# Kernel tuning notes

Hardware: AMD Instinct MI355X
Metric: run time of the kernel (lower is better)

## Reference

```python
import jax, jax.numpy as jnp
import numpy as np

N, M, E, DIM, H = 50000, 50000, 640000, 128, 8
DH = DIM // H
EPS = 1e-5

def _prelu(x, alpha):
    return jnp.where(x >= 0, x, alpha * x)

def setup_inputs() -> dict:
    key0 = jax.random.key(0)
    ks = jax.random.split(key0, 12)
    s = 1.0 / np.sqrt(DIM)
    return {
        "query": jax.random.normal(ks[0], (N, DIM), jnp.float32),
        "key": jax.random.normal(ks[1], (M, DIM), jnp.float32),
        "value": jax.random.normal(ks[2], (M, DIM), jnp.float32),
        "query_idx": jax.random.randint(ks[3], (E,), 0, N),
        "key_idx": jax.random.randint(ks[4], (E,), 0, M),
        "Wq": jax.random.normal(ks[5], (DIM, DIM), jnp.float32) * s,
        "bq": jnp.zeros((DIM,), jnp.float32),
        "Wk": jax.random.normal(ks[6], (DIM, DIM), jnp.float32) * s,
        "bk": jnp.zeros((DIM,), jnp.float32),
        "Wv": jax.random.normal(ks[7], (DIM, DIM), jnp.float32) * s,
        "bv": jnp.zeros((DIM,), jnp.float32),
        "Wp": jax.random.normal(ks[8], (DIM, DIM), jnp.float32) * s,
        "bp": jnp.zeros((DIM,), jnp.float32),
        "a": jax.random.normal(ks[9], (1, H, DH), jnp.float32) * 0.1,
        "alpha": jnp.full((1,), 0.25, jnp.float32),
        "gamma": jnp.ones((DIM,), jnp.float32),
        "beta": jnp.zeros((DIM,), jnp.float32),
    }

def reference(query, key, value, query_idx, key_idx, Wq, bq, Wk, bk, Wv, bv, Wp, bp, a, alpha, gamma, beta):
    n = query.shape[0]
    # projections (node-level, then gather per edge; linear commutes with gather)
    Qq = query @ Wq + bq            # [N, DIM]
    Kq = query @ Wk + bk            # [N, DIM] (self-attn key)
    Kk = key @ Wk + bk              # [M, DIM]
    Vq = query @ Wv + bv            # [N, DIM]
    Vv = value @ Wv + bv            # [M, DIM]
    # self-attention score per query node: [N, H, 1]
    attn_qq = (a * _prelu(Qq + Kq, alpha).reshape(n, H, DH)).sum(-1, keepdims=True)
    # per-edge additive attention score: [E, H, 1]
    e_feat = _prelu(Qq[query_idx] + Kk[key_idx], alpha)
    attn_e = (a * e_feat.reshape(-1, H, DH)).sum(-1, keepdims=True)
    # stable softmax over irregular query groups (include self)
    max_attn = jax.lax.stop_gradient(attn_qq.at[query_idx].max(attn_e))
    exp_qq = jnp.exp(attn_qq - max_attn)                 # [N, H, 1]
    exp_e = jnp.exp(attn_e - max_attn[query_idx])        # [E, H, 1]
    denom = exp_qq.at[query_idx].add(exp_e)              # [N, H, 1]
    denom = jnp.where(denom == 0, 1.0, denom)
    # weighted value scatter-sum (value_idx == key_idx)
    msg = exp_qq * Vq.reshape(n, H, DH)
    msg = msg.at[query_idx].add(exp_e * Vv[key_idx].reshape(-1, H, DH))
    out = (msg / denom).reshape(n, DIM) @ Wp + bp
    res = query + out
    mu = res.mean(-1, keepdims=True)
    var = res.var(-1, keepdims=True)
    return gamma * (res - mu) / jnp.sqrt(var + EPS) + beta
```

## Files before the change

### kernel.cpp

```cpp
#include <hip/hip_runtime.h>
#include <math.h>

#define DIM 128
#define NH 8
#define LN_EPS 1e-5f

using bf16x8 = __attribute__((ext_vector_type(8))) short;
using f32x4  = __attribute__((ext_vector_type(4))) float;

__device__ __forceinline__ float prelu_f(float x, float al) { return x >= 0.f ? x : al * x; }

__device__ __forceinline__ short f2bf(float f) {
    unsigned u = __float_as_uint(f);
    unsigned r = (u + 0x7fffu + ((u >> 16) & 1u)) >> 16;
    return (short)r;
}
__device__ __forceinline__ float bflo(unsigned u) { return __uint_as_float(u << 16); }
__device__ __forceinline__ float bfhi(unsigned u) { return __uint_as_float(u & 0xffff0000u); }

__device__ __forceinline__ unsigned cvt_pk_bf16(float lo, float hi) {
    unsigned r;
    asm("v_cvt_pk_bf16_f32 %0, %1, %2" : "=v"(r) : "v"(lo), "v"(hi));
    return r;
}

__device__ __forceinline__ float swz_xor1(float x) {
    return __int_as_float(__builtin_amdgcn_ds_swizzle(__float_as_int(x), 0x041F));
}
__device__ __forceinline__ float swz_xor2(float x) {
    return __int_as_float(__builtin_amdgcn_ds_swizzle(__float_as_int(x), 0x081F));
}
__device__ __forceinline__ float swz_xor4(float x) {
    return __int_as_float(__builtin_amdgcn_ds_swizzle(__float_as_int(x), 0x101F));
}
__device__ __forceinline__ float swz_xor8(float x) {
    return __int_as_float(__builtin_amdgcn_ds_swizzle(__float_as_int(x), 0x201F));
}

__global__ __launch_bounds__(256) void pack_w_kernel(
    const float* __restrict__ W0, const float* __restrict__ W1,
    const float* __restrict__ W2, const float* __restrict__ W3,
    short* __restrict__ P0, short* __restrict__ P1,
    short* __restrict__ P2, short* __restrict__ P3)
{
    const int id = blockIdx.x * 256 + threadIdx.x;
    const int mat = id >> 11;
    const int rem = id & 2047;
    const int ks = rem >> 9;
    const int ct = (rem >> 6) & 7;
    const int lane = rem & 63;
    const int lr = lane & 15, lg = lane >> 4;
    const float* W = mat == 0 ? W0 : mat == 1 ? W1 : mat == 2 ? W2 : W3;
    short* P = mat == 0 ? P0 : mat == 1 ? P1 : mat == 2 ? P2 : P3;
    short v[8];
    #pragma unroll
    for (int r = 0; r < 8; ++r)
        v[r] = f2bf(W[(ks * 32 + lg * 8 + r) * DIM + ct * 16 + lr]);
    *(bf16x8*)&P[(size_t)((ks * 8 + ct) * 64 + lane) * 8] = *(bf16x8*)v;
}

__global__ __launch_bounds__(256) void proj_query_mfma(
    const float* __restrict__ query,
    const short* __restrict__ Wqp, const short* __restrict__ Wkp, const short* __restrict__ Wvp,
    const float* __restrict__ bq, const float* __restrict__ bk, const float* __restrict__ bv,
    const float* __restrict__ avec, const float* __restrict__ alpha_p,
    float* __restrict__ QV32, float* __restrict__ attnqq, int N)
{
    __shared__ float lds[4][16][130];
    const int wid = threadIdx.x >> 6, lane = threadIdx.x & 63;
    const int row0 = (blockIdx.x * 4 + wid) * 16;
    if (row0 >= N) return;
    const int lr = lane & 15, lg = lane >> 4;

    bf16x8 afrag[4];
    const int arow = row0 + lr;
    const bool rowok = arow < N;
    #pragma unroll
    for (int ks = 0; ks < 4; ++ks) {
        float t[8] = {0.f,0.f,0.f,0.f,0.f,0.f,0.f,0.f};
        if (rowok) {
            *(float4*)&t[0] = *(const float4*)&query[(size_t)arow * DIM + ks * 32 + lg * 8];
            *(float4*)&t[4] = *(const float4*)&query[(size_t)arow * DIM + ks * 32 + lg * 8 + 4];
        }
        bf16x8 a;
        #pragma unroll
        for (int j = 0; j < 8; ++j) a[j] = f2bf(t[j]);
        afrag[ks] = a;
    }

    f32x4 accQ[8], accK[8], accV[8];
    #pragma unroll
    for (int ct = 0; ct < 8; ++ct) { accQ[ct] = (f32x4)0.f; accK[ct] = (f32x4)0.f; accV[ct] = (f32x4)0.f; }

    #pragma unroll
    for (int ks = 0; ks < 4; ++ks) {
        #pragma unroll
        for (int ct = 0; ct < 8; ++ct) {
            const size_t bo = (size_t)((ks * 8 + ct) * 64 + lane) * 8;
            const bf16x8 bq_ = *(const bf16x8*)&Wqp[bo];
            const bf16x8 bk_ = *(const bf16x8*)&Wkp[bo];
            const bf16x8 bv_ = *(const bf16x8*)&Wvp[bo];
            accQ[ct] = __builtin_amdgcn_mfma_f32_16x16x32_bf16(afrag[ks], bq_, accQ[ct], 0, 0, 0);
            accK[ct] = __builtin_amdgcn_mfma_f32_16x16x32_bf16(afrag[ks], bk_, accK[ct], 0, 0, 0);
            accV[ct] = __builtin_amdgcn_mfma_f32_16x16x32_bf16(afrag[ks], bv_, accV[ct], 0, 0, 0);
        }
    }

    const float al = alpha_p[0];
    #pragma unroll
    for (int ct = 0; ct < 8; ++ct) {
        const int col = ct * 16 + lr;
        const float bqv = bq[col], bkv = bk[col], av = avec[col];
        #pragma unroll
        for (int r = 0; r < 4; ++r) {
            const int grow = row0 + lg * 4 + r;
            const float qv = accQ[ct][r] + bqv;
            const float kv = accK[ct][r] + bkv;
            lds[wid][lg * 4 + r][col] = qv;
            float part = av * prelu_f(qv + kv, al);
            part += swz_xor1(part);
            part += swz_xor2(part);
            part += swz_xor4(part);
            part += swz_xor8(part);
            if (lr == 0 && grow < N) attnqq[(size_t)grow * NH + ct] = part;
        }
    }
    const int cl = lane * 2;
    #pragma unroll
    for (int rr = 0; rr < 16; ++rr) {
        const int grow = row0 + rr;
        if (grow < N)
            *(float2*)&QV32[(size_t)grow * 256 + cl] = *(const float2*)&lds[wid][rr][cl];
    }
    #pragma unroll
    for (int ct = 0; ct < 8; ++ct) {
        const int col = ct * 16 + lr;
        const float bvv = bv[col];
        #pragma unroll
        for (int r = 0; r < 4; ++r)
            lds[wid][lg * 4 + r][col] = accV[ct][r] + bvv;
    }
    #pragma unroll
    for (int rr = 0; rr < 16; ++rr) {
        const int grow = row0 + rr;
        if (grow < N)
            *(float2*)&QV32[(size_t)grow * 256 + 128 + cl] = *(const float2*)&lds[wid][rr][cl];
    }
}

__global__ __launch_bounds__(256) void proj_kv_mfma(
    const float* __restrict__ key, const float* __restrict__ value,
    const short* __restrict__ Wkp, const short* __restrict__ Wvp,
    const float* __restrict__ bk, const float* __restrict__ bv,
    short* __restrict__ KV16, int M)
{
    __shared__ float lds[4][16][130];
    const int wid = threadIdx.x >> 6, lane = threadIdx.x & 63;
    const int row0 = (blockIdx.x * 4 + wid) * 16;
    if (row0 >= M) return;
    const int lr = lane & 15, lg = lane >> 4;

    bf16x8 afK[4], afV[4];
    const int arow = row0 + lr;
    const bool rowok = arow < M;
    #pragma unroll
    for (int ks = 0; ks < 4; ++ks) {
        float tk[8] = {0.f,0.f,0.f,0.f,0.f,0.f,0.f,0.f};
        float tv[8] = {0.f,0.f,0.f,0.f,0.f,0.f,0.f,0.f};
        if (rowok) {
            *(float4*)&tk[0] = *(const float4*)&key[(size_t)arow * DIM + ks * 32 + lg * 8];
            *(float4*)&tk[4] = *(const float4*)&key[(size_t)arow * DIM + ks * 32 + lg * 8 + 4];
            *(float4*)&tv[0] = *(const float4*)&value[(size_t)arow * DIM + ks * 32 + lg * 8];
            *(float4*)&tv[4] = *(const float4*)&value[(size_t)arow * DIM + ks * 32 + lg * 8 + 4];
        }
        bf16x8 a, b;
        #pragma unroll
        for (int j = 0; j < 8; ++j) { a[j] = f2bf(tk[j]); b[j] = f2bf(tv[j]); }
        afK[ks] = a; afV[ks] = b;
    }

    f32x4 accK[8], accV[8];
    #pragma unroll
    for (int ct = 0; ct < 8; ++ct) { accK[ct] = (f32x4)0.f; accV[ct] = (f32x4)0.f; }

    #pragma unroll
    for (int ks = 0; ks < 4; ++ks) {
        #pragma unroll
        for (int ct = 0; ct < 8; ++ct) {
            const size_t bo = (size_t)((ks * 8 + ct) * 64 + lane) * 8;
            const bf16x8 bk_ = *(const bf16x8*)&Wkp[bo];
            const bf16x8 bv_ = *(const bf16x8*)&Wvp[bo];
            accK[ct] = __builtin_amdgcn_mfma_f32_16x16x32_bf16(afK[ks], bk_, accK[ct], 0, 0, 0);
            accV[ct] = __builtin_amdgcn_mfma_f32_16x16x32_bf16(afV[ks], bv_, accV[ct], 0, 0, 0);
        }
    }

    const int cl = lane * 2;
    #pragma unroll
    for (int ct = 0; ct < 8; ++ct) {
        const int col = ct * 16 + lr;
        const float bkv = bk[col];
        #pragma unroll
        for (int r = 0; r < 4; ++r)
            lds[wid][lg * 4 + r][col] = accK[ct][r] + bkv;
    }
    #pragma unroll
    for (int rr = 0; rr < 16; ++rr) {
        const int grow = row0 + rr;
        if (grow < M) {
            const float2 q = *(const float2*)&lds[wid][rr][cl];
            *(unsigned*)&KV16[(size_t)grow * 256 + cl] = cvt_pk_bf16(q.x, q.y);
        }
    }
    #pragma unroll
    for (int ct = 0; ct < 8; ++ct) {
        const int col = ct * 16 + lr;
        const float bvv = bv[col];
        #pragma unroll
        for (int r = 0; r < 4; ++r)
            lds[wid][lg * 4 + r][col] = accV[ct][r] + bvv;
    }
    #pragma unroll
    for (int rr = 0; rr < 16; ++rr) {
        const int grow = row0 + rr;
        if (grow < M) {
            const float2 q = *(const float2*)&lds[wid][rr][cl];
            *(unsigned*)&KV16[(size_t)grow * 256 + 128 + cl] = cvt_pk_bf16(q.x, q.y);
        }
    }
}

__global__ void hist_kernel(const int* __restrict__ qidx, int* __restrict__ counts, int E)
{
    for (int e = blockIdx.x * blockDim.x + threadIdx.x; e < E; e += gridDim.x * blockDim.x)
        atomicAdd(&counts[qidx[e]], 1);
}

__global__ __launch_bounds__(256) void scan1_kernel(const int* __restrict__ counts,
                                                    int* __restrict__ bsum, int N)
{
    __shared__ int sh[256];
    int i = blockIdx.x * 256 + threadIdx.x;
    sh[threadIdx.x] = (i < N) ? counts[i] : 0;
    __syncthreads();
    #pragma unroll
    for (int off = 128; off; off >>= 1) {
        if (threadIdx.x < off) sh[threadIdx.x] += sh[threadIdx.x + off];
        __syncthreads();
    }
    if (threadIdx.x == 0) bsum[blockIdx.x] = sh[0];
}

__global__ __launch_bounds__(256) void scan2_kernel(const int* __restrict__ bsum,
                                                    int* __restrict__ boff, int B)
{
    int t = threadIdx.x;
    if (B > 256) {
        if (t == 0) { int run = 0; for (int i = 0; i < B; ++i) { int v = bsum[i]; boff[i] = run; run += v; } }
        return;
    }
    __shared__ int sh[256];
    int v = (t < B) ? bsum[t] : 0;
    sh[t] = v;
    __syncthreads();
    for (int off = 1; off < 256; off <<= 1) {
        int x = (t >= off) ? sh[t - off] : 0;
        __syncthreads();
        sh[t] += x;
        __syncthreads();
    }
    if (t < B) boff[t] = sh[t] - v;
}

__global__ __launch_bounds__(256) void scan3_kernel(const int* __restrict__ counts,
                                                    const int* __restrict__ boff,
                                                    int* __restrict__ offsets,
                                                    int* __restrict__ cursor,
                                                    int N, int E)
{
    __shared__ int sh[256];
    int t = threadIdx.x;
    int i = blockIdx.x * 256 + t;
    int v = (i < N) ? counts[i] : 0;
    sh[t] = v;
    __syncthreads();
    for (int off = 1; off < 256; off <<= 1) {
        int x = (t >= off) ? sh[t - off] : 0;
        __syncthreads();
        sh[t] += x;
        __syncthreads();
    }
    int base = boff[blockIdx.x];
    if (i < N) {
        int o = base + sh[t] - v;
        offsets[i] = o;
        cursor[i] = o;
    }
    if (i == 0) offsets[N] = E;
}

__global__ void fill_kernel(const int* __restrict__ qidx, const int* __restrict__ kidx,
                            int* __restrict__ cursor, int* __restrict__ ksorted, int E)
{
    for (int e = blockIdx.x * blockDim.x + threadIdx.x; e < E; e += gridDim.x * blockDim.x) {
        int q = qidx[e];
        int pos = atomicAdd(&cursor[q], 1);
        ksorted[pos] = kidx[e];
    }
}

__global__ __launch_bounds__(256) void edge_agg_kernel(
    const float* __restrict__ QV32, const float* __restrict__ attnqq,
    const short* __restrict__ KV16,
    const int* __restrict__ ksorted, const int* __restrict__ offsets,
    const float* __restrict__ avec, const float* __restrict__ alpha_p,
    short* __restrict__ msgn16, int N)
{
    const int wid = threadIdx.x >> 6;
    const int lane = threadIdx.x & 63;
    const int n = blockIdx.x * 4 + wid;
    if (n >= N) return;

    const float al = alpha_p[0];
    const int d0 = lane * 2;
    const int h = lane >> 3;

    const float2 qq = *(const float2*)&QV32[(size_t)n * 256 + d0];
    const float2 vq = *(const float2*)&QV32[(size_t)n * 256 + 128 + d0];
    const float2 av = *(const float2*)&avec[d0];
    const float c1x = av.x * (1.f + al) * 0.5f, c2x = av.x * (1.f - al) * 0.5f;
    const float c1y = av.y * (1.f + al) * 0.5f, c2y = av.y * (1.f - al) * 0.5f;

    float m = attnqq[(size_t)n * NH + h];
    float den = 1.f;
    float accx = vq.x, accy = vq.y;

    const int p0 = offsets[n], p1 = offsets[n + 1];

    #define SCORE(kk2, sout)                                                     \
        {                                                                        \
            const float x0 = qq.x + bflo(kk2);                                   \
            const float x1 = qq.y + bfhi(kk2);                                   \
            float s_ = fmaf(c1x, x0, fmaf(c2x, __builtin_fabsf(x0),              \
                       fmaf(c1y, x1, c2y * __builtin_fabsf(x1))));               \
            s_ += swz_xor1(s_);                                                  \
            s_ += swz_xor2(s_);                                                  \
            s_ += swz_xor4(s_);                                                  \
            sout = s_;                                                           \
        }
    #define SLOW(s_, vv_)                                                        \
        {                                                                        \
            const float nm = fmaxf(m, s_);                                       \
            const float c = __expf(m - nm);                                      \
            const float w = __expf(s_ - nm);                                     \
            den = den * c + w;                                                   \
            accx = fmaf(accx, c, w * bflo(vv_));                                 \
            accy = fmaf(accy, c, w * bfhi(vv_));                                 \
            m = nm;                                                              \
        }

    int p = p0;
    const int nrem = (p1 - p0) & 3;
    for (int i = 0; i < nrem; ++i, ++p) {
        const int ki = ksorted[p];
        const unsigned kk2 = *(const unsigned*)&KV16[(size_t)ki * 256 + d0];
        const unsigned vv2 = *(const unsigned*)&KV16[(size_t)ki * 256 + 128 + d0];
        float s;
        SCORE(kk2, s);
        const float d = s - m;
        if (__any(d > 8.f)) {
            SLOW(s, vv2);
        } else {
            const float w = __expf(d);
            den += w;
            accx = fmaf(w, bflo(vv2), accx);
            accy = fmaf(w, bfhi(vv2), accy);
        }
    }

    for (; p < p1; p += 4) {
        const int ka = ksorted[p],     kb = ksorted[p + 1];
        const int kc = ksorted[p + 2], kd = ksorted[p + 3];
        const unsigned kka = *(const unsigned*)&KV16[(size_t)ka * 256 + d0];
        const unsigned kkb = *(const unsigned*)&KV16[(size_t)kb * 256 + d0];
        const unsigned kkc = *(const unsigned*)&KV16[(size_t)kc * 256 + d0];
        const unsigned kkd = *(const unsigned*)&KV16[(size_t)kd * 256 + d0];
        const unsigned vva = *(const unsigned*)&KV16[(size_t)ka * 256 + 128 + d0];
        const unsigned vvb = *(const unsigned*)&KV16[(size_t)kb * 256 + 128 + d0];
        const unsigned vvc = *(const unsigned*)&KV16[(size_t)kc * 256 + 128 + d0];
        const unsigned vvd = *(const unsigned*)&KV16[(size_t)kd * 256 + 128 + d0];
        float sa, sb, sc, sd;
        SCORE(kka, sa);
        SCORE(kkb, sb);
        SCORE(kkc, sc);
        SCORE(kkd, sd);
        const float da = sa - m, db = sb - m, dc = sc - m, dd = sd - m;
        const float dmax = fmaxf(fmaxf(da, db), fmaxf(dc, dd));
        if (__any(dmax > 8.f)) {
            SLOW(sa, vva);
            SLOW(sb, vvb);
            SLOW(sc, vvc);
            SLOW(sd, vvd);
        } else {
            const float wa = __expf(da);
            const float wb = __expf(db);
            const float wc = __expf(dc);
            const float wd = __expf(dd);
            den += (wa + wb) + (wc + wd);
            accx = fmaf(wa, bflo(vva), fmaf(wb, bflo(vvb),
                   fmaf(wc, bflo(vvc), fmaf(wd, bflo(vvd), accx))));
            accy = fmaf(wa, bfhi(vva), fmaf(wb, bfhi(vvb),
                   fmaf(wc, bfhi(vvc), fmaf(wd, bfhi(vvd), accy))));
        }
    }
    #undef SCORE
    #undef SLOW

    const float inv = 1.f / den;
    *(unsigned*)&msgn16[(size_t)n * DIM + d0] = cvt_pk_bf16(accx * inv, accy * inv);
}

__global__ __launch_bounds__(256) void out_ln_mfma(
    const short* __restrict__ msgn16, const short* __restrict__ Wpp,
    const float* __restrict__ bp, const float* __restrict__ query,
    const float* __restrict__ gamma, const float* __restrict__ beta,
    float* __restrict__ out, int N)
{
    __shared__ float ys[64][130];
    const int wid = threadIdx.x >> 6, lane = threadIdx.x & 63;
    const int rowbase = blockIdx.x * 64;
    const int row0 = rowbase + wid * 16;
    const int lr = lane & 15, lg = lane >> 4;

    if (row0 < N) {
        bf16x8 afrag[4];
        const int arow = row0 + lr;
        const bool rowok = arow < N;
        #pragma unroll
        for (int ks = 0; ks < 4; ++ks) {
            if (rowok)
                afrag[ks] = *(const bf16x8*)&msgn16[(size_t)arow * DIM + ks * 32 + lg * 8];
            else {
                bf16x8 z;
                #pragma unroll
                for (int j = 0; j < 8; ++j) z[j] = 0;
                afrag[ks] = z;
            }
        }
        f32x4 acc[8];
        #pragma unroll
        for (int ct = 0; ct < 8; ++ct) acc[ct] = (f32x4)0.f;
        #pragma unroll
        for (int ks = 0; ks < 4; ++ks) {
            #pragma unroll
            for (int ct = 0; ct < 8; ++ct) {
                const size_t bo = (size_t)((ks * 8 + ct) * 64 + lane) * 8;
                const bf16x8 b_ = *(const bf16x8*)&Wpp[bo];
                acc[ct] = __builtin_amdgcn_mfma_f32_16x16x32_bf16(afrag[ks], b_, acc[ct], 0, 0, 0);
            }
        }
        #pragma unroll
        for (int ct = 0; ct < 8; ++ct) {
            const int col = ct * 16 + lr;
            const float bpv = bp[col];
            #pragma unroll
            for (int r = 0; r < 4; ++r)
                ys[wid * 16 + lg * 4 + r][col] = acc[ct][r] + bpv;
        }
    }
    __syncthreads();

    for (int rr = 0; rr < 16; ++rr) {
        const int r = wid * 16 + rr;
        const int grow = rowbase + r;
        if (grow >= N) break;
        const float y1 = ys[r][lane], y2 = ys[r][lane + 64];
        const float q1 = query[(size_t)grow * DIM + lane];
        const float q2 = query[(size_t)grow * DIM + lane + 64];
        const float r1 = y1 + q1, r2 = y2 + q2;
        float s = r1 + r2;
        float ss = r1 * r1 + r2 * r2;
        #pragma unroll
        for (int off = 32; off; off >>= 1) {
            s += __shfl_xor(s, off);
            ss += __shfl_xor(ss, off);
        }
        const float mu = s * (1.f / DIM);
        const float var = ss * (1.f / DIM) - mu * mu;
        const float rstd = rsqrtf(var + LN_EPS);
        out[(size_t)grow * DIM + lane] = gamma[lane] * (r1 - mu) * rstd + beta[lane];
        out[(size_t)grow * DIM + lane + 64] = gamma[lane + 64] * (r2 - mu) * rstd + beta[lane + 64];
    }
}

extern "C" void kernel_launch(void* const* d_in, const int* in_sizes, int n_in,
                              void* d_out, int out_size, void* d_ws, size_t ws_size,
                              hipStream_t stream) {
    const float* query = (const float*)d_in[0];
    const float* key   = (const float*)d_in[1];
    const float* value = (const float*)d_in[2];
    const int* query_idx = (const int*)d_in[3];
    const int* key_idx   = (const int*)d_in[4];
    const float* Wq = (const float*)d_in[5];
    const float* bq = (const float*)d_in[6];
    const float* Wk = (const float*)d_in[7];
    const float* bk = (const float*)d_in[8];
    const float* Wv = (const float*)d_in[9];
    const float* bv = (const float*)d_in[10];
    const float* Wp = (const float*)d_in[11];
    const float* bp = (const float*)d_in[12];
    const float* avec  = (const float*)d_in[13];
    const float* alpha = (const float*)d_in[14];
    const float* gamma = (const float*)d_in[15];
    const float* beta  = (const float*)d_in[16];
    float* out = (float*)d_out;

    const int N = in_sizes[0] / DIM;
    const int M = in_sizes[1] / DIM;
    const int E = in_sizes[3];

    float* f = (float*)d_ws;
    float* QV32 = f;    f += (size_t)N * 256;
    float* attnqq = f;  f += (size_t)N * NH;
    short* sp = (short*)f;
    short* KV16 = sp;   sp += (size_t)M * 256;
    short* msgn16 = sp; sp += (size_t)N * DIM;
    short* Wqp = sp;    sp += DIM * DIM;
    short* Wkp = sp;    sp += DIM * DIM;
    short* Wvp = sp;    sp += DIM * DIM;
    short* Wpp = sp;    sp += DIM * DIM;
    int* ip = (int*)(((size_t)sp + 15) & ~(size_t)15);
    int* counts  = ip;  ip += N;
    int* offsets = ip;  ip += N + 1;
    int* cursor  = ip;  ip += N;
    int* bsum    = ip;  ip += 4096;
    int* boff    = ip;  ip += 4096;
    int* ksorted = ip;  ip += E;

    const int B = (N + 255) / 256;

    hipMemsetAsync(counts, 0, (size_t)N * sizeof(int), stream);

    pack_w_kernel<<<32, 256, 0, stream>>>(Wq, Wk, Wv, Wp, Wqp, Wkp, Wvp, Wpp);

    proj_query_mfma<<<(N + 63) / 64, 256, 0, stream>>>(
        query, Wqp, Wkp, Wvp, bq, bk, bv, avec, alpha, QV32, attnqq, N);
    proj_kv_mfma<<<(M + 63) / 64, 256, 0, stream>>>(
        key, value, Wkp, Wvp, bk, bv, KV16, M);

    hist_kernel<<<1024, 256, 0, stream>>>(query_idx, counts, E);
    scan1_kernel<<<B, 256, 0, stream>>>(counts, bsum, N);
    scan2_kernel<<<1, 256, 0, stream>>>(bsum, boff, B);
    scan3_kernel<<<B, 256, 0, stream>>>(counts, boff, offsets, cursor, N, E);
    fill_kernel<<<1024, 256, 0, stream>>>(query_idx, key_idx, cursor, ksorted, E);

    edge_agg_kernel<<<(N + 3) / 4, 256, 0, stream>>>(
        QV32, attnqq, KV16, ksorted, offsets, avec, alpha, msgn16, N);

    out_ln_mfma<<<(N + 63) / 64, 256, 0, stream>>>(
        msgn16, Wpp, bp, query, gamma, beta, out, N);
}
```

Baseline: 228.4 us.

## Fuse setup and projection kernels, store Q/V in bf16, restructure edge aggregation per head

```diff
diff --git a/kernel.cpp b/kernel.cpp
--- a/kernel.cpp
+++ b/kernel.cpp
@@ -4,6 +4,7 @@
 #define DIM 128
 #define NH 8
 #define LN_EPS 1e-5f
+#define NEGINF -3.0e38f
 
 using bf16x8 = __attribute__((ext_vector_type(8))) short;
 using f32x4  = __attribute__((ext_vector_type(4))) float;
@@ -36,204 +37,205 @@
 __device__ __forceinline__ float swz_xor8(float x) {
     return __int_as_float(__builtin_amdgcn_ds_swizzle(__float_as_int(x), 0x201F));
 }
-
-__global__ __launch_bounds__(256) void pack_w_kernel(
+__device__ __forceinline__ float swz_xor16(float x) {
+    return __int_as_float(__builtin_amdgcn_ds_swizzle(__float_as_int(x), 0x401F));
+}
+__device__ __forceinline__ float swz_xor32(float x) {
+    return __shfl_xor(x, 32);
+}
+
+__global__ __launch_bounds__(256) void setup_kernel(
     const float* __restrict__ W0, const float* __restrict__ W1,
     const float* __restrict__ W2, const float* __restrict__ W3,
     short* __restrict__ P0, short* __restrict__ P1,
-    short* __restrict__ P2, short* __restrict__ P3)
-{
-    const int id = blockIdx.x * 256 + threadIdx.x;
-    const int mat = id >> 11;
-    const int rem = id & 2047;
-    const int ks = rem >> 9;
-    const int ct = (rem >> 6) & 7;
-    const int lane = rem & 63;
-    const int lr = lane & 15, lg = lane >> 4;
-    const float* W = mat == 0 ? W0 : mat == 1 ? W1 : mat == 2 ? W2 : W3;
-    short* P = mat == 0 ? P0 : mat == 1 ? P1 : mat == 2 ? P2 : P3;
-    short v[8];
-    #pragma unroll
-    for (int r = 0; r < 8; ++r)
-        v[r] = f2bf(W[(ks * 32 + lg * 8 + r) * DIM + ct * 16 + lr]);
-    *(bf16x8*)&P[(size_t)((ks * 8 + ct) * 64 + lane) * 8] = *(bf16x8*)v;
-}
-
-__global__ __launch_bounds__(256) void proj_query_mfma(
+    short* __restrict__ P2, short* __restrict__ P3,
+    const int* __restrict__ qidx, int* __restrict__ counts, int E)
+{
+    if (blockIdx.x < 32) {
+        const int id = blockIdx.x * 256 + threadIdx.x;
+        const int mat = id >> 11;
+        const int rem = id & 2047;
+        const int ks = rem >> 9;
+        const int ct = (rem >> 6) & 7;
+        const int lane = rem & 63;
+        const int lr = lane & 15, lg = lane >> 4;
+        const float* W = mat == 0 ? W0 : mat == 1 ? W1 : mat == 2 ? W2 : W3;
+        short* P = mat == 0 ? P0 : mat == 1 ? P1 : mat == 2 ? P2 : P3;
+        short v[8];
+        #pragma unroll
+        for (int r = 0; r < 8; ++r)
+            v[r] = f2bf(W[(ks * 32 + lg * 8 + r) * DIM + ct * 16 + lr]);
+        *(bf16x8*)&P[(size_t)((ks * 8 + ct) * 64 + lane) * 8] = *(bf16x8*)v;
+    } else {
+        const int b = blockIdx.x - 32;
+        for (int e = b * 256 + threadIdx.x; e < E; e += 1024 * 256)
+            atomicAdd(&counts[qidx[e]], 1);
+    }
+}
+
+__global__ __launch_bounds__(256) void proj_all_mfma(
     const float* __restrict__ query,
+    const float* __restrict__ key, const float* __restrict__ value,
     const short* __restrict__ Wqp, const short* __restrict__ Wkp, const short* __restrict__ Wvp,
     const float* __restrict__ bq, const float* __restrict__ bk, const float* __restrict__ bv,
     const float* __restrict__ avec, const float* __restrict__ alpha_p,
-    float* __restrict__ QV32, float* __restrict__ attnqq, int N)
+    short* __restrict__ QV16, float* __restrict__ attnqq,
+    short* __restrict__ KV16, int N, int M, int nb)
 {
     __shared__ float lds[4][16][130];
     const int wid = threadIdx.x >> 6, lane = threadIdx.x & 63;
-    const int row0 = (blockIdx.x * 4 + wid) * 16;
-    if (row0 >= N) return;
     const int lr = lane & 15, lg = lane >> 4;
-
-    bf16x8 afrag[4];
-    const int arow = row0 + lr;
-    const bool rowok = arow < N;
-    #pragma unroll
-    for (int ks = 0; ks < 4; ++ks) {
-        float t[8] = {0.f,0.f,0.f,0.f,0.f,0.f,0.f,0.f};
-        if (rowok) {
-            *(float4*)&t[0] = *(const float4*)&query[(size_t)arow * DIM + ks * 32 + lg * 8];
-            *(float4*)&t[4] = *(const float4*)&query[(size_t)arow * DIM + ks * 32 + lg * 8 + 4];
-        }
-        bf16x8 a;
-        #pragma unroll
-        for (int j = 0; j < 8; ++j) a[j] = f2bf(t[j]);
-        afrag[ks] = a;
-    }
-
-    f32x4 accQ[8], accK[8], accV[8];
-    #pragma unroll
-    for (int ct = 0; ct < 8; ++ct) { accQ[ct] = (f32x4)0.f; accK[ct] = (f32x4)0.f; accV[ct] = (f32x4)0.f; }
-
-    #pragma unroll
-    for (int ks = 0; ks < 4; ++ks) {
+    const int cl = lane * 2;
+
+    if ((int)blockIdx.x < nb) {
+        const int row0 = (blockIdx.x * 4 + wid) * 16;
+        if (row0 >= N) return;
+        bf16x8 afrag[4];
+        const int arow = row0 + lr;
+        const bool rowok = arow < N;
+        #pragma unroll
+        for (int ks = 0; ks < 4; ++ks) {
+            float t[8] = {0.f,0.f,0.f,0.f,0.f,0.f,0.f,0.f};
+            if (rowok) {
+                *(float4*)&t[0] = *(const float4*)&query[(size_t)arow * DIM + ks * 32 + lg * 8];
+                *(float4*)&t[4] = *(const float4*)&query[(size_t)arow * DIM + ks * 32 + lg * 8 + 4];
+            }
+            bf16x8 a;
+            #pragma unroll
+            for (int j = 0; j < 8; ++j) a[j] = f2bf(t[j]);
+            afrag[ks] = a;
+        }
+
+        f32x4 accQ[8], accK[8], accV[8];
+        #pragma unroll
+        for (int ct = 0; ct < 8; ++ct) { accQ[ct] = (f32x4)0.f; accK[ct] = (f32x4)0.f; accV[ct] = (f32x4)0.f; }
+        #pragma unroll
+        for (int ks = 0; ks < 4; ++ks) {
+            #pragma unroll
+            for (int ct = 0; ct < 8; ++ct) {
+                const size_t bo = (size_t)((ks * 8 + ct) * 64 + lane) * 8;
+                const bf16x8 bq_ = *(const bf16x8*)&Wqp[bo];
+                const bf16x8 bk_ = *(const bf16x8*)&Wkp[bo];
+                const bf16x8 bv_ = *(const bf16x8*)&Wvp[bo];
+                accQ[ct] = __builtin_amdgcn_mfma_f32_16x16x32_bf16(afrag[ks], bq_, accQ[ct], 0, 0, 0);
+                accK[ct] = __builtin_amdgcn_mfma_f32_16x16x32_bf16(afrag[ks], bk_, accK[ct], 0, 0, 0);
+                accV[ct] = __builtin_amdgcn_mfma_f32_16x16x32_bf16(afrag[ks], bv_, accV[ct], 0, 0, 0);
+            }
+        }
+
+        const float al = alpha_p[0];
         #pragma unroll
         for (int ct = 0; ct < 8; ++ct) {
-            const size_t bo = (size_t)((ks * 8 + ct) * 64 + lane) * 8;
-            const bf16x8 bq_ = *(const bf16x8*)&Wqp[bo];
-            const bf16x8 bk_ = *(const bf16x8*)&Wkp[bo];
-            const bf16x8 bv_ = *(const bf16x8*)&Wvp[bo];
-            accQ[ct] = __builtin_amdgcn_mfma_f32_16x16x32_bf16(afrag[ks], bq_, accQ[ct], 0, 0, 0);
-            accK[ct] = __builtin_amdgcn_mfma_f32_16x16x32_bf16(afrag[ks], bk_, accK[ct], 0, 0, 0);
-            accV[ct] = __builtin_amdgcn_mfma_f32_16x16x32_bf16(afrag[ks], bv_, accV[ct], 0, 0, 0);
-        }
-    }
-
-    const float al = alpha_p[0];
-    #pragma unroll
-    for (int ct = 0; ct < 8; ++ct) {
-        const int col = ct * 16 + lr;
-        const float bqv = bq[col], bkv = bk[col], av = avec[col];
-        #pragma unroll
-        for (int r = 0; r < 4; ++r) {
-            const int grow = row0 + lg * 4 + r;
-            const float qv = accQ[ct][r] + bqv;
-            const float kv = accK[ct][r] + bkv;
-            lds[wid][lg * 4 + r][col] = qv;
-            float part = av * prelu_f(qv + kv, al);
-            part += swz_xor1(part);
-            part += swz_xor2(part);
-            part += swz_xor4(part);
-            part += swz_xor8(part);
-            if (lr == 0 && grow < N) attnqq[(size_t)grow * NH + ct] = part;
-        }
-    }
-    const int cl = lane * 2;
-    #pragma unroll
-    for (int rr = 0; rr < 16; ++rr) {
-        const int grow = row0 + rr;
-        if (grow < N)
-            *(float2*)&QV32[(size_t)grow * 256 + cl] = *(const float2*)&lds[wid][rr][cl];
-    }
-    #pragma unroll
-    for (int ct = 0; ct < 8; ++ct) {
-        const int col = ct * 16 + lr;
-        const float bvv = bv[col];
-        #pragma unroll
-        for (int r = 0; r < 4; ++r)
-            lds[wid][lg * 4 + r][col] = accV[ct][r] + bvv;
-    }
-    #pragma unroll
-    for (int rr = 0; rr < 16; ++rr) {
-        const int grow = row0 + rr;
-        if (grow < N)
-            *(float2*)&QV32[(size_t)grow * 256 + 128 + cl] = *(const float2*)&lds[wid][rr][cl];
-    }
-}
-
-__global__ __launch_bounds__(256) void proj_kv_mfma(
-    const float* __restrict__ key, const float* __restrict__ value,
-    const short* __restrict__ Wkp, const short* __restrict__ Wvp,
-    const float* __restrict__ bk, const float* __restrict__ bv,
-    short* __restrict__ KV16, int M)
-{
-    __shared__ float lds[4][16][130];
-    const int wid = threadIdx.x >> 6, lane = threadIdx.x & 63;
-    const int row0 = (blockIdx.x * 4 + wid) * 16;
-    if (row0 >= M) return;
-    const int lr = lane & 15, lg = lane >> 4;
-
-    bf16x8 afK[4], afV[4];
-    const int arow = row0 + lr;
-    const bool rowok = arow < M;
-    #pragma unroll
-    for (int ks = 0; ks < 4; ++ks) {
-        float tk[8] = {0.f,0.f,0.f,0.f,0.f,0.f,0.f,0.f};
-        float tv[8] = {0.f,0.f,0.f,0.f,0.f,0.f,0.f,0.f};
-        if (rowok) {
-            *(float4*)&tk[0] = *(const float4*)&key[(size_t)arow * DIM + ks * 32 + lg * 8];
-            *(float4*)&tk[4] = *(const float4*)&key[(size_t)arow * DIM + ks * 32 + lg * 8 + 4];
-            *(float4*)&tv[0] = *(const float4*)&value[(size_t)arow * DIM + ks * 32 + lg * 8];
-            *(float4*)&tv[4] = *(const float4*)&value[(size_t)arow * DIM + ks * 32 + lg * 8 + 4];
-        }
-        bf16x8 a, b;
-        #pragma unroll
-        for (int j = 0; j < 8; ++j) { a[j] = f2bf(tk[j]); b[j] = f2bf(tv[j]); }
-        afK[ks] = a; afV[ks] = b;
-    }
-
-    f32x4 accK[8], accV[8];
-    #pragma unroll
-    for (int ct = 0; ct < 8; ++ct) { accK[ct] = (f32x4)0.f; accV[ct] = (f32x4)0.f; }
-
-    #pragma unroll
-    for (int ks = 0; ks < 4; ++ks) {
+            const int col = ct * 16 + lr;
+            const float bqv = bq[col], bkv = bk[col], av = avec[col];
+            #pragma unroll
+            for (int r = 0; r < 4; ++r) {
+                const int grow = row0 + lg * 4 + r;
+                const float qv = accQ[ct][r] + bqv;
+                const float kv = accK[ct][r] + bkv;
+                lds[wid][lg * 4 + r][col] = qv;
+                float part = av * prelu_f(qv + kv, al);
+                part += swz_xor1(part);
+                part += swz_xor2(part);
+                part += swz_xor4(part);
+                part += swz_xor8(part);
+                if (lr == 0 && grow < N) attnqq[(size_t)grow * NH + ct] = part;
+            }
+        }
+        #pragma unroll
+        for (int rr = 0; rr < 16; ++rr) {
+            const int grow = row0 + rr;
+            if (grow < N) {
+                const float2 t = *(const float2*)&lds[wid][rr][cl];
+                *(unsigned*)&QV16[(size_t)grow * 256 + cl] = cvt_pk_bf16(t.x, t.y);
+            }
+        }
         #pragma unroll
         for (int ct = 0; ct < 8; ++ct) {
-            const size_t bo = (size_t)((ks * 8 + ct) * 64 + lane) * 8;
-            const bf16x8 bk_ = *(const bf16x8*)&Wkp[bo];
-            const bf16x8 bv_ = *(const bf16x8*)&Wvp[bo];
-            accK[ct] = __builtin_amdgcn_mfma_f32_16x16x32_bf16(afK[ks], bk_, accK[ct], 0, 0, 0);
-            accV[ct] = __builtin_amdgcn_mfma_f32_16x16x32_bf16(afV[ks], bv_, accV[ct], 0, 0, 0);
-        }
-    }
-
-    const int cl = lane * 2;
-    #pragma unroll
-    for (int ct = 0; ct < 8; ++ct) {
-        const int col = ct * 16 + lr;
-        const float bkv = bk[col];
-        #pragma unroll
-        for (int r = 0; r < 4; ++r)
-            lds[wid][lg * 4 + r][col] = accK[ct][r] + bkv;
-    }
-    #pragma unroll
-    for (int rr = 0; rr < 16; ++rr) {
-        const int grow = row0 + rr;
-        if (grow < M) {
-            const float2 q = *(const float2*)&lds[wid][rr][cl];
-            *(unsigned*)&KV16[(size_t)grow * 256 + cl] = cvt_pk_bf16(q.x, q.y);
-        }
-    }
-    #pragma unroll
-    for (int ct = 0; ct < 8; ++ct) {
-        const int col = ct * 16 + lr;
-        const float bvv = bv[col];
-        #pragma unroll
-        for (int r = 0; r < 4; ++r)
-            lds[wid][lg * 4 + r][col] = accV[ct][r] + bvv;
-    }
-    #pragma unroll
-    for (int rr = 0; rr < 16; ++rr) {
-        const int grow = row0 + rr;
-        if (grow < M) {
-            const float2 q = *(const float2*)&lds[wid][rr][cl];
-            *(unsigned*)&KV16[(size_t)grow * 256 + 128 + cl] = cvt_pk_bf16(q.x, q.y);
-        }
-    }
-}
-
-__global__ void hist_kernel(const int* __restrict__ qidx, int* __restrict__ counts, int E)
-{
-    for (int e = blockIdx.x * blockDim.x + threadIdx.x; e < E; e += gridDim.x * blockDim.x)
-        atomicAdd(&counts[qidx[e]], 1);
+            const int col = ct * 16 + lr;
+            const float bvv = bv[col];
+            #pragma unroll
+            for (int r = 0; r < 4; ++r)
+                lds[wid][lg * 4 + r][col] = accV[ct][r] + bvv;
+        }
+        #pragma unroll
+        for (int rr = 0; rr < 16; ++rr) {
+            const int grow = row0 + rr;
+            if (grow < N) {
+                const float2 t = *(const float2*)&lds[wid][rr][cl];
+                *(unsigned*)&QV16[(size_t)grow * 256 + 128 + cl] = cvt_pk_bf16(t.x, t.y);
+            }
+        }
+    } else {
+        const int row0 = (((int)blockIdx.x - nb) * 4 + wid) * 16;
+        if (row0 >= M) return;
+        bf16x8 afK[4], afV[4];
+        const int arow = row0 + lr;
+        const bool rowok = arow < M;
+        #pragma unroll
+        for (int ks = 0; ks < 4; ++ks) {
+            float tk[8] = {0.f,0.f,0.f,0.f,0.f,0.f,0.f,0.f};
+            float tv[8] = {0.f,0.f,0.f,0.f,0.f,0.f,0.f,0.f};
+            if (rowok) {
+                *(float4*)&tk[0] = *(const float4*)&key[(size_t)arow * DIM + ks * 32 + lg * 8];
+                *(float4*)&tk[4] = *(const float4*)&key[(size_t)arow * DIM + ks * 32 + lg * 8 + 4];
+                *(float4*)&tv[0] = *(const float4*)&value[(size_t)arow * DIM + ks * 32 + lg * 8];
+                *(float4*)&tv[4] = *(const float4*)&value[(size_t)arow * DIM + ks * 32 + lg * 8 + 4];
+            }
+            bf16x8 a, b;
+            #pragma unroll
+            for (int j = 0; j < 8; ++j) { a[j] = f2bf(tk[j]); b[j] = f2bf(tv[j]); }
+            afK[ks] = a; afV[ks] = b;
+        }
+
+        f32x4 accK[8], accV[8];
+        #pragma unroll
+        for (int ct = 0; ct < 8; ++ct) { accK[ct] = (f32x4)0.f; accV[ct] = (f32x4)0.f; }
+        #pragma unroll
+        for (int ks = 0; ks < 4; ++ks) {
+            #pragma unroll
+            for (int ct = 0; ct < 8; ++ct) {
+                const size_t bo = (size_t)((ks * 8 + ct) * 64 + lane) * 8;
+                const bf16x8 bk_ = *(const bf16x8*)&Wkp[bo];
+                const bf16x8 bv_ = *(const bf16x8*)&Wvp[bo];
+                accK[ct] = __builtin_amdgcn_mfma_f32_16x16x32_bf16(afK[ks], bk_, accK[ct], 0, 0, 0);
+                accV[ct] = __builtin_amdgcn_mfma_f32_16x16x32_bf16(afV[ks], bv_, accV[ct], 0, 0, 0);
+            }
+        }
+
+        #pragma unroll
+        for (int ct = 0; ct < 8; ++ct) {
+            const int col = ct * 16 + lr;
+            const float bkv = bk[col];
+            #pragma unroll
+            for (int r = 0; r < 4; ++r)
+                lds[wid][lg * 4 + r][col] = accK[ct][r] + bkv;
+        }
+        #pragma unroll
+        for (int rr = 0; rr < 16; ++rr) {
+            const int grow = row0 + rr;
+            if (grow < M) {
+                const float2 t = *(const float2*)&lds[wid][rr][cl];
+                *(unsigned*)&KV16[(size_t)grow * 256 + cl] = cvt_pk_bf16(t.x, t.y);
+            }
+        }
+        #pragma unroll
+        for (int ct = 0; ct < 8; ++ct) {
+            const int col = ct * 16 + lr;
+            const float bvv = bv[col];
+            #pragma unroll
+            for (int r = 0; r < 4; ++r)
+                lds[wid][lg * 4 + r][col] = accV[ct][r] + bvv;
+        }
+        #pragma unroll
+        for (int rr = 0; rr < 16; ++rr) {
+            const int grow = row0 + rr;
+            if (grow < M) {
+                const float2 t = *(const float2*)&lds[wid][rr][cl];
+                *(unsigned*)&KV16[(size_t)grow * 256 + 128 + cl] = cvt_pk_bf16(t.x, t.y);
+            }
+        }
+    }
 }
 
 __global__ __launch_bounds__(256) void scan1_kernel(const int* __restrict__ counts,
@@ -310,7 +312,7 @@
 }
 
 __global__ __launch_bounds__(256) void edge_agg_kernel(
-    const float* __restrict__ QV32, const float* __restrict__ attnqq,
+    const short* __restrict__ QV16, const float* __restrict__ attnqq,
     const short* __restrict__ KV16,
     const int* __restrict__ ksorted, const int* __restrict__ offsets,
     const float* __restrict__ avec, const float* __restrict__ alpha_p,
@@ -321,103 +323,146 @@
     const int n = blockIdx.x * 4 + wid;
     if (n >= N) return;
 
+    const int h = lane & 7;
+    const int e = lane >> 3;
     const float al = alpha_p[0];
-    const int d0 = lane * 2;
-    const int h = lane >> 3;
-
-    const float2 qq = *(const float2*)&QV32[(size_t)n * 256 + d0];
-    const float2 vq = *(const float2*)&QV32[(size_t)n * 256 + 128 + d0];
-    const float2 av = *(const float2*)&avec[d0];
-    const float c1x = av.x * (1.f + al) * 0.5f, c2x = av.x * (1.f - al) * 0.5f;
-    const float c1y = av.y * (1.f + al) * 0.5f, c2y = av.y * (1.f - al) * 0.5f;
+
+    float c1[16], c2[16];
+    {
+        const float s1 = (1.f + al) * 0.5f, s2 = (1.f - al) * 0.5f;
+        #pragma unroll
+        for (int j = 0; j < 4; ++j) {
+            const float4 a4 = *(const float4*)&avec[h * 16 + j * 4];
+            c1[j*4+0] = a4.x * s1; c2[j*4+0] = a4.x * s2;
+            c1[j*4+1] = a4.y * s1; c2[j*4+1] = a4.y * s2;
+            c1[j*4+2] = a4.z * s1; c2[j*4+2] = a4.z * s2;
+            c1[j*4+3] = a4.w * s1; c2[j*4+3] = a4.w * s2;
+        }
+    }
+
+    const size_t qb = (size_t)n * 256 + h * 16;
+    float q[16];
+    {
+        const uint4 lo = *(const uint4*)&QV16[qb];
+        const uint4 hi = *(const uint4*)&QV16[qb + 8];
+        const unsigned qd[8] = {lo.x, lo.y, lo.z, lo.w, hi.x, hi.y, hi.z, hi.w};
+        #pragma unroll
+        for (int j = 0; j < 8; ++j) { q[2*j] = bflo(qd[j]); q[2*j+1] = bfhi(qd[j]); }
+    }
+
+    float acc[16];
+    float den;
+    if (e == 0) {
+        const uint4 lo = *(const uint4*)&QV16[qb + 128];
+        const uint4 hi = *(const uint4*)&QV16[qb + 136];
+        const unsigned vd[8] = {lo.x, lo.y, lo.z, lo.w, hi.x, hi.y, hi.z, hi.w};
+        #pragma unroll
+        for (int j = 0; j < 8; ++j) { acc[2*j] = bflo(vd[j]); acc[2*j+1] = bfhi(vd[j]); }
+        den = 1.f;
+    } else {
+        #pragma unroll
+        for (int d = 0; d < 16; ++d) acc[d] = 0.f;
+        den = 0.f;
+    }
 
     float m = attnqq[(size_t)n * NH + h];
-    float den = 1.f;
-    float accx = vq.x, accy = vq.y;
-
     const int p0 = offsets[n], p1 = offsets[n + 1];
-
-    #define SCORE(kk2, sout)                                                     \
-        {                                                                        \
-            const float x0 = qq.x + bflo(kk2);                                   \
-            const float x1 = qq.y + bfhi(kk2);                                   \
-            float s_ = fmaf(c1x, x0, fmaf(c2x, __builtin_fabsf(x0),              \
-                       fmaf(c1y, x1, c2y * __builtin_fabsf(x1))));               \
-            s_ += swz_xor1(s_);                                                  \
-            s_ += swz_xor2(s_);                                                  \
-            s_ += swz_xor4(s_);                                                  \
-            sout = s_;                                                           \
-        }
-    #define SLOW(s_, vv_)                                                        \
-        {                                                                        \
-            const float nm = fmaxf(m, s_);                                       \
-            const float c = __expf(m - nm);                                      \
-            const float w = __expf(s_ - nm);                                     \
-            den = den * c + w;                                                   \
-            accx = fmaf(accx, c, w * bflo(vv_));                                 \
-            accy = fmaf(accy, c, w * bfhi(vv_));                                 \
-            m = nm;                                                              \
-        }
-
-    int p = p0;
-    const int nrem = (p1 - p0) & 3;
-    for (int i = 0; i < nrem; ++i, ++p) {
-        const int ki = ksorted[p];
-        const unsigned kk2 = *(const unsigned*)&KV16[(size_t)ki * 256 + d0];
-        const unsigned vv2 = *(const unsigned*)&KV16[(size_t)ki * 256 + 128 + d0];
-        float s;
-        SCORE(kk2, s);
-        const float d = s - m;
-        if (__any(d > 8.f)) {
-            SLOW(s, vv2);
+    bool div = false;
+
+    int idx = p0 + e;
+    bool valid = idx < p1;
+    int ki = valid ? ksorted[idx] : 0;
+
+    for (int base = p0; base < p1; base += 8) {
+        const int cki = ki;
+        const bool cval = valid;
+        const int nidx = base + 8 + e;
+        valid = nidx < p1;
+        ki = valid ? ksorted[nidx] : 0;
+
+        const size_t kb = (size_t)cki * 256 + h * 16;
+        const uint4 klo = *(const uint4*)&KV16[kb];
+        const uint4 khi = *(const uint4*)&KV16[kb + 8];
+        const uint4 vlo = *(const uint4*)&KV16[kb + 128];
+        const uint4 vhi = *(const uint4*)&KV16[kb + 136];
+        const unsigned kd[8] = {klo.x, klo.y, klo.z, klo.w, khi.x, khi.y, khi.z, khi.w};
+        const unsigned vd[8] = {vlo.x, vlo.y, vlo.z, vlo.w, vhi.x, vhi.y, vhi.z, vhi.w};
+
+        float sA = 0.f, sB = 0.f;
+        #pragma unroll
+        for (int j = 0; j < 8; ++j) {
+            const float x0 = q[2*j]   + bflo(kd[j]);
+            const float x1 = q[2*j+1] + bfhi(kd[j]);
+            sA = fmaf(c1[2*j],   x0, fmaf(c2[2*j],   __builtin_fabsf(x0), sA));
+            sB = fmaf(c1[2*j+1], x1, fmaf(c2[2*j+1], __builtin_fabsf(x1), sB));
+        }
+        const float s = cval ? (sA + sB) : NEGINF;
+        const float d_ = s - m;
+
+        if (__any(d_ > 8.f)) {
+            div = true;
+            const float nm = fmaxf(m, s);
+            const float c = __expf(m - nm);
+            const float w = __expf(s - nm);
+            den = den * c + w;
+            #pragma unroll
+            for (int j = 0; j < 8; ++j) {
+                acc[2*j]   = fmaf(acc[2*j],   c, w * bflo(vd[j]));
+                acc[2*j+1] = fmaf(acc[2*j+1], c, w * bfhi(vd[j]));
+            }
+            m = nm;
         } else {
-            const float w = __expf(d);
+            const float w = __expf(d_);
             den += w;
-            accx = fmaf(w, bflo(vv2), accx);
-            accy = fmaf(w, bfhi(vv2), accy);
-        }
-    }
-
-    for (; p < p1; p += 4) {
-        const int ka = ksorted[p],     kb = ksorted[p + 1];
-        const int kc = ksorted[p + 2], kd = ksorted[p + 3];
-        const unsigned kka = *(const unsigned*)&KV16[(size_t)ka * 256 + d0];
-        const unsigned kkb = *(const unsigned*)&KV16[(size_t)kb * 256 + d0];
-        const unsigned kkc = *(const unsigned*)&KV16[(size_t)kc * 256 + d0];
-        const unsigned kkd = *(const unsigned*)&KV16[(size_t)kd * 256 + d0];
-        const unsigned vva = *(const unsigned*)&KV16[(size_t)ka * 256 + 128 + d0];
-        const unsigned vvb = *(const unsigned*)&KV16[(size_t)kb * 256 + 128 + d0];
-        const unsigned vvc = *(const unsigned*)&KV16[(size_t)kc * 256 + 128 + d0];
-        const unsigned vvd = *(const unsigned*)&KV16[(size_t)kd * 256 + 128 + d0];
-        float sa, sb, sc, sd;
-        SCORE(kka, sa);
-        SCORE(kkb, sb);
-        SCORE(kkc, sc);
-        SCORE(kkd, sd);
-        const float da = sa - m, db = sb - m, dc = sc - m, dd = sd - m;
-        const float dmax = fmaxf(fmaxf(da, db), fmaxf(dc, dd));
-        if (__any(dmax > 8.f)) {
-            SLOW(sa, vva);
-            SLOW(sb, vvb);
-            SLOW(sc, vvc);
-            SLOW(sd, vvd);
-        } else {
-            const float wa = __expf(da);
-            const float wb = __expf(db);
-            const float wc = __expf(dc);
-            const float wd = __expf(dd);
-            den += (wa + wb) + (wc + wd);
-            accx = fmaf(wa, bflo(vva), fmaf(wb, bflo(vvb),
-                   fmaf(wc, bflo(vvc), fmaf(wd, bflo(vvd), accx))));
-            accy = fmaf(wa, bfhi(vva), fmaf(wb, bfhi(vvb),
-                   fmaf(wc, bfhi(vvc), fmaf(wd, bfhi(vvd), accy))));
-        }
-    }
-    #undef SCORE
-    #undef SLOW
-
-    const float inv = 1.f / den;
-    *(unsigned*)&msgn16[(size_t)n * DIM + d0] = cvt_pk_bf16(accx * inv, accy * inv);
+            #pragma unroll
+            for (int j = 0; j < 8; ++j) {
+                acc[2*j]   = fmaf(w, bflo(vd[j]), acc[2*j]);
+                acc[2*j+1] = fmaf(w, bfhi(vd[j]), acc[2*j+1]);
+            }
+        }
+    }
+
+    #define MERGE_ROUND(SWZ)                                    \
+        {                                                       \
+            const float m2 = SWZ(m);                            \
+            const float den2 = SWZ(den);                        \
+            const float nm = fmaxf(m, m2);                      \
+            const float ca = __expf(m - nm);                    \
+            const float cb = __expf(m2 - nm);                   \
+            den = den * ca + den2 * cb;                         \
+            _Pragma("unroll")                                   \
+            for (int d = 0; d < 16; ++d)                        \
+                acc[d] = acc[d] * ca + SWZ(acc[d]) * cb;        \
+            m = nm;                                             \
+        }
+    #define SUM_ROUND(SWZ)                                      \
+        {                                                       \
+            den += SWZ(den);                                    \
+            _Pragma("unroll")                                   \
+            for (int d = 0; d < 16; ++d) acc[d] += SWZ(acc[d]); \
+        }
+
+    if (div) {
+        MERGE_ROUND(swz_xor8);
+        MERGE_ROUND(swz_xor16);
+        MERGE_ROUND(swz_xor32);
+    } else {
+        SUM_ROUND(swz_xor8);
+        SUM_ROUND(swz_xor16);
+        SUM_ROUND(swz_xor32);
+    }
+    #undef MERGE_ROUND
+    #undef SUM_ROUND
+
+    if (e == 0) {
+        const float inv = 1.f / den;
+        unsigned u[8];
+        #pragma unroll
+        for (int j = 0; j < 8; ++j)
+            u[j] = cvt_pk_bf16(acc[2*j] * inv, acc[2*j+1] * inv);
+        *(uint4*)&msgn16[(size_t)n * DIM + h * 16]     = make_uint4(u[0], u[1], u[2], u[3]);
+        *(uint4*)&msgn16[(size_t)n * DIM + h * 16 + 8] = make_uint4(u[4], u[5], u[6], u[7]);
+    }
 }
 
 __global__ __launch_bounds__(256) void out_ln_mfma(
@@ -520,9 +565,9 @@
     const int E = in_sizes[3];
 
     float* f = (float*)d_ws;
-    float* QV32 = f;    f += (size_t)N * 256;
     float* attnqq = f;  f += (size_t)N * NH;
     short* sp = (short*)f;
+    short* QV16 = sp;   sp += (size_t)N * 256;
     short* KV16 = sp;   sp += (size_t)M * 256;
     short* msgn16 = sp; sp += (size_t)N * DIM;
     short* Wqp = sp;    sp += DIM * DIM;
@@ -538,24 +583,25 @@
     int* ksorted = ip;  ip += E;
 
     const int B = (N + 255) / 256;
+    const int nb = (N + 63) / 64;
+    const int mb = (M + 63) / 64;
 
     hipMemsetAsync(counts, 0, (size_t)N * sizeof(int), stream);
 
-    pack_w_kernel<<<32, 256, 0, stream>>>(Wq, Wk, Wv, Wp, Wqp, Wkp, Wvp, Wpp);
-
-    proj_query_mfma<<<(N + 63) / 64, 256, 0, stream>>>(
-        query, Wqp, Wkp, Wvp, bq, bk, bv, avec, alpha, QV32, attnqq, N);
-    proj_kv_mfma<<<(M + 63) / 64, 256, 0, stream>>>(
-        key, value, Wkp, Wvp, bk, bv, KV16, M);
-
-    hist_kernel<<<1024, 256, 0, stream>>>(query_idx, counts, E);
+    setup_kernel<<<1056, 256, 0, stream>>>(Wq, Wk, Wv, Wp, Wqp, Wkp, Wvp, Wpp,
+                                           query_idx, counts, E);
+
     scan1_kernel<<<B, 256, 0, stream>>>(counts, bsum, N);
     scan2_kernel<<<1, 256, 0, stream>>>(bsum, boff, B);
     scan3_kernel<<<B, 256, 0, stream>>>(counts, boff, offsets, cursor, N, E);
     fill_kernel<<<1024, 256, 0, stream>>>(query_idx, key_idx, cursor, ksorted, E);
 
+    proj_all_mfma<<<nb + mb, 256, 0, stream>>>(
+        query, key, value, Wqp, Wkp, Wvp, bq, bk, bv, avec, alpha,
+        QV16, attnqq, KV16, N, M, nb);
+
     edge_agg_kernel<<<(N + 3) / 4, 256, 0, stream>>>(
-        QV32, attnqq, KV16, ksorted, offsets, avec, alpha, msgn16, N);
+        QV16, attnqq, KV16, ksorted, offsets, avec, alpha, msgn16, N);
 
     out_ln_mfma<<<(N + 63) / 64, 256, 0, stream>>>(
         msgn16, Wpp, bp, query, gamma, beta, out, N);
```

After: 224.4 us. No clear change (-1.7%).
